# Kernel optimization log

Hardware: AMD Instinct MI355X
Metric: run time of the kernel (lower is better)

Reference implementation:

```python
import jax, jax.numpy as jnp
import numpy as np

B, L, D, H = 4, 2048, 1024, 16
d = D // H  # head_dim = 64
EPS = 1e-5
ROPE_BASE = 10000.0


def _rope_tables(seq_len, dim):
    inv_freq = 1.0 / (ROPE_BASE ** (jnp.arange(0, dim, 2, dtype=jnp.float32) / dim))
    t = jnp.arange(seq_len, dtype=jnp.float32)
    freqs = jnp.outer(t, inv_freq)                  # (L, d/2)
    emb = jnp.concatenate([freqs, freqs], axis=-1)  # (L, d)
    return jnp.cos(emb), jnp.sin(emb)


def _rotate_half(x):
    x1, x2 = jnp.split(x, 2, axis=-1)
    return jnp.concatenate([-x2, x1], axis=-1)


def setup_inputs() -> dict:
    key = jax.random.key(0)
    ks = jax.random.split(key, 5)
    x = jax.random.normal(ks[0], (B, L, D), dtype=jnp.float32)
    attn_mask = jnp.ones((B, 1, L, L), dtype=jnp.float32)
    conversion_mask = jax.random.uniform(ks[1], (B, L), dtype=jnp.float32)
    Wqkuv = jax.random.normal(ks[2], (D, 4 * D), dtype=jnp.float32) * (1.0 / np.sqrt(D))
    Wout = jax.random.normal(ks[3], (D, D), dtype=jnp.float32) * (1.0 / np.sqrt(D))
    ln_gamma = jnp.ones((d,), dtype=jnp.float32)
    ln_beta = jnp.zeros((d,), dtype=jnp.float32)
    conv_bias = jax.random.normal(ks[4], (H,), dtype=jnp.float32) * 0.02
    return {"x": x, "attn_mask": attn_mask, "conversion_mask": conversion_mask,
            "Wqkuv": Wqkuv, "Wout": Wout, "ln_gamma": ln_gamma,
            "ln_beta": ln_beta, "conv_bias": conv_bias}


def reference(x, attn_mask, conversion_mask, Wqkuv, Wout, ln_gamma, ln_beta, conv_bias):
    # qkuv projection with SiLU
    qkuv = jax.nn.silu(jnp.einsum('bld,de->ble', x, Wqkuv))  # (B, L, 4D)
    q, k, v, u = jnp.split(qkuv, 4, axis=-1)
    # reshape to (B, H, L, d)
    to_heads = lambda t: t.reshape(B, L, H, d).transpose(0, 2, 1, 3)
    q, k, v, u = map(to_heads, (q, k, v, u))
    # RoPE
    cos, sin = _rope_tables(L, d)            # (L, d)
    cos = cos[None, None]                    # (1,1,L,d)
    sin = sin[None, None]
    q = q * cos + _rotate_half(q) * sin
    k = k * cos + _rotate_half(k) * sin
    # scores + conversion bias + SiLU + multiplicative mask
    scores = jnp.einsum('bhld,bhmd->bhlm', q, k) / jnp.sqrt(jnp.float32(d))
    scores = scores + conversion_mask[:, None, None, :] * conv_bias[None, :, None, None]
    scores = jax.nn.silu(scores)
    scores = scores * attn_mask
    # attend, LayerNorm over head_dim, SiLU-gate with u
    attn_out = jnp.einsum('bhlm,bhmd->bhld', scores, v)
    mu = jnp.mean(attn_out, axis=-1, keepdims=True)
    var = jnp.var(attn_out, axis=-1, keepdims=True)
    attn_out = (attn_out - mu) / jnp.sqrt(var + EPS) * ln_gamma + ln_beta
    attn_out = attn_out * u
    attn_out = attn_out.transpose(0, 2, 1, 3).reshape(B, L, D)
    return jnp.einsum('bld,de->ble', attn_out, Wout)
```

## Files before the change

### kernel.cpp

```cpp
#include <hip/hip_runtime.h>
#include <math.h>
#include <stdint.h>

#define B_ 4
#define L_ 2048
#define D_ 1024
#define H_ 16

typedef __attribute__((ext_vector_type(4))) float f32x4;
typedef __attribute__((ext_vector_type(2))) float f32x2;
typedef __attribute__((ext_vector_type(8))) short s16x8;
typedef __attribute__((ext_vector_type(4))) short s16x4;
typedef __attribute__((ext_vector_type(4))) unsigned short u16x4;
typedef __attribute__((ext_vector_type(4))) unsigned int u32x4;
typedef __attribute__((ext_vector_type(2))) __bf16 bf16x2;

__device__ __forceinline__ unsigned short f2bf(float f) {
  unsigned int u = __float_as_uint(f);
  u += 0x7fffu + ((u >> 16) & 1u);
  return (unsigned short)(u >> 16);
}
__device__ __forceinline__ float b2f(unsigned short s) {
  return __uint_as_float(((unsigned int)s) << 16);
}
__device__ __forceinline__ unsigned int pk2(float a, float b) {
  f32x2 v;
  v[0] = a;
  v[1] = b;
  bf16x2 r = __builtin_convertvector(v, bf16x2);
  return __builtin_bit_cast(unsigned int, r);
}
__device__ __forceinline__ float silu_fast(float v) {
  return v * __builtin_amdgcn_rcpf(1.0f + __expf(-v));
}
__device__ __forceinline__ void gl_lds16(const void* g, void* l) {
  __builtin_amdgcn_global_load_lds(
      (__attribute__((address_space(1))) void*)(uintptr_t)g,
      (__attribute__((address_space(3))) void*)(uint32_t)(uintptr_t)l, 16, 0, 0);
}

__global__ __launch_bounds__(256) void conv_x(const float* __restrict__ x,
                                              unsigned short* __restrict__ xb, int n4) {
  int i = blockIdx.x * 256 + threadIdx.x;
  if (i < n4) {
    f32x4 v = *(const f32x4*)(x + (size_t)i * 4);
    u16x4 o;
#pragma unroll
    for (int j = 0; j < 4; ++j) o[j] = f2bf(v[j]);
    *(u16x4*)(xb + (size_t)i * 4) = o;
  }
}

__global__ __launch_bounds__(256) void trans_w(const float* __restrict__ W,
                                               unsigned short* __restrict__ Wt,
                                               int K, int N) {
  __shared__ float T[64][65];
  const int k0 = blockIdx.y * 64, n0 = blockIdx.x * 64;
  const int tid = threadIdx.x;
#pragma unroll
  for (int i = 0; i < 16; ++i) {
    int e = tid + i * 256;
    int r = e >> 6, c = e & 63;
    T[r][c] = W[(size_t)(k0 + r) * N + n0 + c];
  }
  __syncthreads();
#pragma unroll
  for (int i = 0; i < 16; ++i) {
    int e = tid + i * 256;
    int r = e >> 6, c = e & 63;
    Wt[(size_t)(n0 + r) * K + k0 + c] = f2bf(T[c][r]);
  }
}

__global__ __launch_bounds__(256) void rope_tab(f32x2* __restrict__ tab) {
  int i = blockIdx.x * 256 + threadIdx.x;
  int l = i >> 5, j = i & 31;
  float inv = expf(-(float)j * (9.210340371976184f / 32.0f));
  float ang = (float)l * inv;
  f32x2 cs;
  cs[0] = cosf(ang);
  cs[1] = sinf(ang);
  tab[i] = cs;
}

template <int MODE>
__global__ __launch_bounds__(256) void gemm_bf16(const unsigned short* __restrict__ A,
                                                 const unsigned short* __restrict__ Bt,
                                                 void* __restrict__ Cp,
                                                 int M, int N, int K) {
  alignas(16) __shared__ unsigned short As[128][32];
  alignas(16) __shared__ unsigned short Bs[128][32];
  const int tid = threadIdx.x;
  const int lane = tid & 63, w = tid >> 6;
  const int quad = lane >> 4, l15 = lane & 15;
  const int wr = w >> 1, wc = w & 1;
  const int m0 = blockIdx.y * 128, n0 = blockIdx.x * 128;
  const int srow = lane >> 2;
  const int schunk = (lane & 3) ^ ((lane >> 3) & 3);
  const int fcol = (quad ^ ((l15 >> 1) & 3)) * 8;
  f32x4 acc[4][4] = {};
  for (int k0 = 0; k0 < K; k0 += 32) {
    __syncthreads();
#pragma unroll
    for (int i = 0; i < 2; ++i) {
      int r0 = (w * 2 + i) * 16;
      gl_lds16(A + (size_t)(m0 + r0 + srow) * K + k0 + schunk * 8, &As[r0][0]);
      gl_lds16(Bt + (size_t)(n0 + r0 + srow) * K + k0 + schunk * 8, &Bs[r0][0]);
    }
    __syncthreads();
    s16x8 af[4], bf[4];
#pragma unroll
    for (int mi = 0; mi < 4; ++mi) af[mi] = *(const s16x8*)&As[wr * 64 + mi * 16 + l15][fcol];
#pragma unroll
    for (int nj = 0; nj < 4; ++nj) bf[nj] = *(const s16x8*)&Bs[wc * 64 + nj * 16 + l15][fcol];
#pragma unroll
    for (int mi = 0; mi < 4; ++mi)
#pragma unroll
      for (int nj = 0; nj < 4; ++nj)
        acc[mi][nj] = __builtin_amdgcn_mfma_f32_16x16x32_bf16(af[mi], bf[nj], acc[mi][nj], 0, 0, 0);
  }
#pragma unroll
  for (int mi = 0; mi < 4; ++mi)
#pragma unroll
    for (int nj = 0; nj < 4; ++nj)
#pragma unroll
      for (int reg = 0; reg < 4; ++reg) {
        int rg = m0 + wr * 64 + mi * 16 + quad * 4 + reg;
        int cg = n0 + wc * 64 + nj * 16 + l15;
        float v = acc[mi][nj][reg];
        if (MODE == 1) {
          ((unsigned short*)Cp)[(size_t)rg * N + cg] = f2bf(silu_fast(v));
        } else {
          ((float*)Cp)[(size_t)rg * N + cg] = v;
        }
      }
}

__global__ __launch_bounds__(256) void rope_conv(unsigned short* __restrict__ qk,
                                                 unsigned short* __restrict__ vt,
                                                 const f32x2* __restrict__ tab) {
  alignas(16) __shared__ unsigned short Vsh[64][72];
  const int tid = threadIdx.x;
  const int bh = blockIdx.y, b = bh >> 4, h = bh & 15;
  const int l0 = blockIdx.x * 64;
#pragma unroll
  for (int i = 0; i < 2; ++i) {
    int p = tid + i * 256;
    int row = p >> 3, c4 = p & 7;
    int l = l0 + row;
    size_t base = (size_t)(b * L_ + l) * 4096 + h * 64 + c4 * 4;
#pragma unroll
    for (int t = 0; t < 2; ++t) {
      size_t o = base + (size_t)t * 1024;
      u16x4 lo = *(u16x4*)(qk + o);
      u16x4 hi = *(u16x4*)(qk + o + 32);
      u16x4 nlo, nhi;
#pragma unroll
      for (int jj = 0; jj < 4; ++jj) {
        f32x2 cs = tab[l * 32 + c4 * 4 + jj];
        float fl = b2f(lo[jj]), fh = b2f(hi[jj]);
        nlo[jj] = f2bf(fl * cs[0] - fh * cs[1]);
        nhi[jj] = f2bf(fh * cs[0] + fl * cs[1]);
      }
      *(u16x4*)(qk + o) = nlo;
      *(u16x4*)(qk + o + 32) = nhi;
    }
  }
#pragma unroll
  for (int i = 0; i < 2; ++i) {
    int ch = tid + i * 256;
    int row = ch >> 3, c8 = ch & 7;
    *(s16x8*)&Vsh[row][c8 * 8] =
        *(const s16x8*)(qk + (size_t)(b * L_ + l0 + row) * 4096 + 2048 + h * 64 + c8 * 8);
  }
  __syncthreads();
#pragma unroll
  for (int i = 0; i < 2; ++i) {
    int ch = tid + i * 256;
    int drow = ch >> 3, c8 = ch & 7;
    s16x8 o;
#pragma unroll
    for (int jj = 0; jj < 8; ++jj) {
      int pos = c8 * 8 + jj;
      int g = pos >> 5, p = pos & 31;
      int lk = g * 32 + ((p >> 2) & 1) * 16 + ((p >> 3) & 3) * 4 + (p & 3);
      o[jj] = (short)Vsh[lk][drow];
    }
    *(s16x8*)(vt + (size_t)(bh * 64 + drow) * 2048 + l0 + c8 * 8) = o;
  }
}

__global__ __launch_bounds__(256) void attn_mfma(
    const unsigned short* __restrict__ qk, const unsigned short* __restrict__ vt,
    const float* __restrict__ amask, const float* __restrict__ cmask,
    const float* __restrict__ cbias, const float* __restrict__ gamma,
    const float* __restrict__ beta, unsigned short* __restrict__ attng) {
  alignas(16) __shared__ unsigned short Ks[64][64];
  alignas(16) __shared__ unsigned short Vts[64][64];
  const int tid = threadIdx.x;
  const int lane = tid & 63, w = tid >> 6;
  const int quad = lane >> 4, l15 = lane & 15;
  const int bh = blockIdx.y, b = bh >> 4, h = bh & 15;
  const int l0 = blockIdx.x * 128;
  const float cb = cbias[h];
  const int srow = lane >> 3;
  const int schunk = (lane & 7) ^ srow;

  s16x8 qf[2][2];
  const float* abase[2];
#pragma unroll
  for (int qs = 0; qs < 2; ++qs) {
    int qg = l0 + w * 32 + qs * 16 + l15;
#pragma unroll
    for (int s = 0; s < 2; ++s)
      qf[qs][s] = *(const s16x8*)(qk + (size_t)(b * L_ + qg) * 4096 + h * 64 + s * 32 + quad * 8);
    abase[qs] = amask + ((size_t)b * L_ + qg) * L_;
  }
  const float* cbase = cmask + (size_t)b * L_;

  f32x4 oacc[2][4] = {};

  for (int m0 = 0; m0 < L_; m0 += 64) {
    __syncthreads();
#pragma unroll
    for (int i = 0; i < 2; ++i) {
      int r0 = w * 16 + i * 8;
      gl_lds16(qk + (size_t)(b * L_ + m0 + r0 + srow) * 4096 + 1024 + h * 64 + schunk * 8,
               &Ks[r0][0]);
      gl_lds16(vt + (size_t)(bh * 64 + r0 + srow) * 2048 + m0 + schunk * 8, &Vts[r0][0]);
    }
    f32x4 cmcb[4], am4[2][4];
#pragma unroll
    for (int kt = 0; kt < 4; ++kt)
      cmcb[kt] = *(const f32x4*)(cbase + m0 + kt * 16 + quad * 4) * cb;
#pragma unroll
    for (int qs = 0; qs < 2; ++qs)
#pragma unroll
      for (int kt = 0; kt < 4; ++kt)
        am4[qs][kt] = *(const f32x4*)(abase[qs] + m0 + kt * 16 + quad * 4);
    __syncthreads();

    f32x4 sacc[2][4] = {};
#pragma unroll
    for (int s = 0; s < 2; ++s) {
      s16x8 kf[4];
#pragma unroll
      for (int kt = 0; kt < 4; ++kt)
        kf[kt] = *(const s16x8*)&Ks[kt * 16 + l15][((s * 4 + quad) ^ (l15 & 7)) * 8];
#pragma unroll
      for (int qs = 0; qs < 2; ++qs)
#pragma unroll
        for (int kt = 0; kt < 4; ++kt)
          sacc[qs][kt] = __builtin_amdgcn_mfma_f32_16x16x32_bf16(kf[kt], qf[qs][s],
                                                                 sacc[qs][kt], 0, 0, 0);
    }

    s16x8 pf[2][2];
#pragma unroll
    for (int qs = 0; qs < 2; ++qs)
#pragma unroll
      for (int t = 0; t < 2; ++t) {
        u32x4 pw;
#pragma unroll
        for (int half = 0; half < 2; ++half) {
          int kt = 2 * t + half;
          float x[4];
#pragma unroll
          for (int r = 0; r < 4; ++r) {
            float v = fmaf(sacc[qs][kt][r], 0.125f, cmcb[kt][r]);
            v = silu_fast(v);
            x[r] = v * am4[qs][kt][r];
          }
          pw[half * 2 + 0] = pk2(x[0], x[1]);
          pw[half * 2 + 1] = pk2(x[2], x[3]);
        }
        pf[qs][t] = __builtin_bit_cast(s16x8, pw);
      }

#pragma unroll
    for (int dt = 0; dt < 4; ++dt)
#pragma unroll
      for (int t = 0; t < 2; ++t) {
        s16x8 vf = *(const s16x8*)&Vts[dt * 16 + l15][((t * 4 + quad) ^ (l15 & 7)) * 8];
#pragma unroll
        for (int qs = 0; qs < 2; ++qs)
          oacc[qs][dt] = __builtin_amdgcn_mfma_f32_16x16x32_bf16(pf[qs][t], vf,
                                                                 oacc[qs][dt], 0, 0, 0);
      }
  }

#pragma unroll
  for (int qs = 0; qs < 2; ++qs) {
    float sm[4], sq[4];
#pragma unroll
    for (int reg = 0; reg < 4; ++reg) {
      float s1 = 0.f, s2 = 0.f;
#pragma unroll
      for (int dt = 0; dt < 4; ++dt) {
        float v = oacc[qs][dt][reg];
        s1 += v;
        s2 += v * v;
      }
      sm[reg] = s1;
      sq[reg] = s2;
    }
#pragma unroll
    for (int m = 1; m < 16; m <<= 1) {
#pragma unroll
      for (int reg = 0; reg < 4; ++reg) {
        sm[reg] += __shfl_xor(sm[reg], m);
        sq[reg] += __shfl_xor(sq[reg], m);
      }
    }
    float mu[4], rs[4];
#pragma unroll
    for (int reg = 0; reg < 4; ++reg) {
      mu[reg] = sm[reg] * (1.0f / 64.0f);
      float var = sq[reg] * (1.0f / 64.0f) - mu[reg] * mu[reg];
      rs[reg] = rsqrtf(var + 1e-5f);
    }
#pragma unroll
    for (int dt = 0; dt < 4; ++dt) {
      float g = gamma[dt * 16 + l15], be = beta[dt * 16 + l15];
#pragma unroll
      for (int reg = 0; reg < 4; ++reg) {
        int rowg = l0 + w * 32 + qs * 16 + quad * 4 + reg;
        int colg = dt * 16 + l15;
        float v = (oacc[qs][dt][reg] - mu[reg]) * rs[reg] * g + be;
        float u = b2f(qk[(size_t)(b * L_ + rowg) * 4096 + 3072 + h * 64 + colg]);
        attng[(size_t)(b * L_ + rowg) * 1024 + h * 64 + colg] = f2bf(v * u);
      }
    }
  }
}

extern "C" void kernel_launch(void* const* d_in, const int* in_sizes, int n_in,
                              void* d_out, int out_size, void* d_ws, size_t ws_size,
                              hipStream_t stream) {
  const float* x = (const float*)d_in[0];
  const float* amask = (const float*)d_in[1];
  const float* cmask = (const float*)d_in[2];
  const float* Wqkuv = (const float*)d_in[3];
  const float* Wout = (const float*)d_in[4];
  const float* gamma = (const float*)d_in[5];
  const float* beta = (const float*)d_in[6];
  const float* cbias = (const float*)d_in[7];
  float* out = (float*)d_out;

  char* ws = (char*)d_ws;
  unsigned short* qkuv_bf = (unsigned short*)ws;
  unsigned short* vt = (unsigned short*)(ws + ((size_t)64 << 20));
  unsigned short* xbf = (unsigned short*)(ws + ((size_t)80 << 20));
  unsigned short* Wt = (unsigned short*)(ws + ((size_t)96 << 20));
  unsigned short* Wot = (unsigned short*)(ws + ((size_t)104 << 20));
  unsigned short* attng = (unsigned short*)(ws + ((size_t)106 << 20));
  f32x2* tab = (f32x2*)(ws + ((size_t)122 << 20));

  conv_x<<<8192, 256, 0, stream>>>(x, xbf, (B_ * L_ * D_) / 4);
  trans_w<<<dim3(4096 / 64, 1024 / 64), 256, 0, stream>>>(Wqkuv, Wt, 1024, 4096);
  trans_w<<<dim3(1024 / 64, 1024 / 64), 256, 0, stream>>>(Wout, Wot, 1024, 1024);
  rope_tab<<<(L_ * 32) / 256, 256, 0, stream>>>(tab);

  gemm_bf16<1><<<dim3(4096 / 128, 8192 / 128), 256, 0, stream>>>(xbf, Wt, qkuv_bf,
                                                                 B_ * L_, 4 * D_, D_);
  rope_conv<<<dim3(L_ / 64, B_ * H_), 256, 0, stream>>>(qkuv_bf, vt, tab);
  attn_mfma<<<dim3(L_ / 128, B_ * H_), 256, 0, stream>>>(qkuv_bf, vt, amask, cmask, cbias,
                                                         gamma, beta, attng);
  gemm_bf16<0><<<dim3(1024 / 128, 8192 / 128), 256, 0, stream>>>(attng, Wot, out,
                                                                 B_ * L_, D_, D_);
}
```

Measured before the change: 462.6 us.

## Rewrite bf16 GEMM as 256x256 double-buffered tile with XCD swizzle and setprio

The GEMM moves from a 128x128 tile with BK=32 and 256 threads to a 256x256 tile with BK=64, 512 threads and double-buffered LDS. The next K tile is prefetched while MFMAs run, and workgroup IDs are swizzled across groups of eight for cache locality. s_setprio wraps the MFMA blocks in both the GEMM and the attention kernel. The goal is to hide global-load latency and raise MFMA utilisation, at the cost of more LDS (128KB) and registers. The output GEMM now launches only 128 blocks, which may underfill the GPU.

Measured after the change: 458.8 us. About the same (-0.8%).

```diff
diff --git a/kernel.cpp b/kernel.cpp
--- a/kernel.cpp
+++ b/kernel.cpp
@@ -84,50 +84,97 @@
 }
 
 template <int MODE>
-__global__ __launch_bounds__(256) void gemm_bf16(const unsigned short* __restrict__ A,
+__global__ __launch_bounds__(512) void gemm_bf16(const unsigned short* __restrict__ A,
                                                  const unsigned short* __restrict__ Bt,
                                                  void* __restrict__ Cp,
                                                  int M, int N, int K) {
-  alignas(16) __shared__ unsigned short As[128][32];
-  alignas(16) __shared__ unsigned short Bs[128][32];
+  alignas(16) __shared__ unsigned short Ash[2][256][64];
+  alignas(16) __shared__ unsigned short Bsh[2][256][64];
   const int tid = threadIdx.x;
   const int lane = tid & 63, w = tid >> 6;
   const int quad = lane >> 4, l15 = lane & 15;
-  const int wr = w >> 1, wc = w & 1;
-  const int m0 = blockIdx.y * 128, n0 = blockIdx.x * 128;
-  const int srow = lane >> 2;
-  const int schunk = (lane & 3) ^ ((lane >> 3) & 3);
-  const int fcol = (quad ^ ((l15 >> 1) & 3)) * 8;
-  f32x4 acc[4][4] = {};
-  for (int k0 = 0; k0 < K; k0 += 32) {
-    __syncthreads();
-#pragma unroll
-    for (int i = 0; i < 2; ++i) {
-      int r0 = (w * 2 + i) * 16;
-      gl_lds16(A + (size_t)(m0 + r0 + srow) * K + k0 + schunk * 8, &As[r0][0]);
-      gl_lds16(Bt + (size_t)(n0 + r0 + srow) * K + k0 + schunk * 8, &Bs[r0][0]);
-    }
-    __syncthreads();
-    s16x8 af[4], bf[4];
-#pragma unroll
-    for (int mi = 0; mi < 4; ++mi) af[mi] = *(const s16x8*)&As[wr * 64 + mi * 16 + l15][fcol];
-#pragma unroll
-    for (int nj = 0; nj < 4; ++nj) bf[nj] = *(const s16x8*)&Bs[wc * 64 + nj * 16 + l15][fcol];
-#pragma unroll
-    for (int mi = 0; mi < 4; ++mi)
-#pragma unroll
-      for (int nj = 0; nj < 4; ++nj)
-        acc[mi][nj] = __builtin_amdgcn_mfma_f32_16x16x32_bf16(af[mi], bf[nj], acc[mi][nj], 0, 0, 0);
-  }
-#pragma unroll
-  for (int mi = 0; mi < 4; ++mi)
-#pragma unroll
-    for (int nj = 0; nj < 4; ++nj)
+  const int wm = w >> 2, wn = w & 3;
+  const int nwg = gridDim.x * gridDim.y;
+  const int wgid = blockIdx.y * gridDim.x + blockIdx.x;
+  const int swz = (wgid & 7) * (nwg >> 3) + (wgid >> 3);
+  const int m0 = (swz / gridDim.x) * 256, n0 = (swz % gridDim.x) * 256;
+
+  const int s_sub = lane >> 3;
+  const int s_src = (lane & 7) ^ s_sub;
+  auto stage = [&](const unsigned short* __restrict__ G, int row0, int k0,
+                   unsigned short (*dst)[64]) {
+#pragma unroll
+    for (int j = 0; j < 4; ++j) {
+      int r = j * 64 + w * 8 + s_sub;
+      gl_lds16(G + (size_t)(row0 + r) * K + k0 + s_src * 8, &dst[j * 64 + w * 8][0]);
+    }
+  };
+
+  f32x4 acc[8][4] = {};
+  const int NT = K / 64;
+
+  stage(A, m0, 0, Ash[0]);
+  stage(Bt, n0, 0, Bsh[0]);
+  asm volatile("s_waitcnt vmcnt(0)" ::: "memory");
+  __builtin_amdgcn_s_barrier();
+  __builtin_amdgcn_sched_barrier(0);
+
+  for (int t = 0; t < NT; ++t) {
+    const int c = t & 1;
+#pragma unroll
+    for (int p = 0; p < 4; ++p) {
+      const int qa = p & 1, qb = p >> 1;
+      s16x8 af[4][2], bf[2][2];
+#pragma unroll
+      for (int i = 0; i < 4; ++i)
+#pragma unroll
+        for (int ks = 0; ks < 2; ++ks)
+          af[i][ks] = *(const s16x8*)&Ash[c][wm * 128 + (qa * 4 + i) * 16 + l15]
+                                           [((ks * 4 + quad) ^ (l15 & 7)) * 8];
+#pragma unroll
+      for (int jn = 0; jn < 2; ++jn)
+#pragma unroll
+        for (int ks = 0; ks < 2; ++ks)
+          bf[jn][ks] = *(const s16x8*)&Bsh[c][wn * 64 + (qb * 2 + jn) * 16 + l15]
+                                            [((ks * 4 + quad) ^ (l15 & 7)) * 8];
+      if (t + 1 < NT) {
+        if (p == 0) stage(A, m0, (t + 1) * 64, Ash[c ^ 1]);
+        if (p == 1) stage(Bt, n0, (t + 1) * 64, Bsh[c ^ 1]);
+      }
+      __builtin_amdgcn_sched_barrier(0);
+      __builtin_amdgcn_s_barrier();
+      __builtin_amdgcn_sched_barrier(0);
+      __builtin_amdgcn_s_setprio(1);
+#pragma unroll
+      for (int i = 0; i < 4; ++i)
+#pragma unroll
+        for (int jn = 0; jn < 2; ++jn)
+#pragma unroll
+          for (int ks = 0; ks < 2; ++ks)
+            acc[qa * 4 + i][qb * 2 + jn] = __builtin_amdgcn_mfma_f32_16x16x32_bf16(
+                af[i][ks], bf[jn][ks], acc[qa * 4 + i][qb * 2 + jn], 0, 0, 0);
+      __builtin_amdgcn_s_setprio(0);
+      if (p < 3) {
+        __builtin_amdgcn_s_barrier();
+        __builtin_amdgcn_sched_barrier(0);
+      }
+    }
+    if (t + 1 < NT) {
+      asm volatile("s_waitcnt vmcnt(0)" ::: "memory");
+    }
+    __builtin_amdgcn_s_barrier();
+    __builtin_amdgcn_sched_barrier(0);
+  }
+
+#pragma unroll
+  for (int fm = 0; fm < 8; ++fm)
+#pragma unroll
+    for (int fn = 0; fn < 4; ++fn)
 #pragma unroll
       for (int reg = 0; reg < 4; ++reg) {
-        int rg = m0 + wr * 64 + mi * 16 + quad * 4 + reg;
-        int cg = n0 + wc * 64 + nj * 16 + l15;
-        float v = acc[mi][nj][reg];
+        int rg = m0 + wm * 128 + fm * 16 + quad * 4 + reg;
+        int cg = n0 + wn * 64 + fn * 16 + l15;
+        float v = acc[fm][fn][reg];
         if (MODE == 1) {
           ((unsigned short*)Cp)[(size_t)rg * N + cg] = f2bf(silu_fast(v));
         } else {
@@ -247,12 +294,14 @@
 #pragma unroll
       for (int kt = 0; kt < 4; ++kt)
         kf[kt] = *(const s16x8*)&Ks[kt * 16 + l15][((s * 4 + quad) ^ (l15 & 7)) * 8];
+      __builtin_amdgcn_s_setprio(1);
 #pragma unroll
       for (int qs = 0; qs < 2; ++qs)
 #pragma unroll
         for (int kt = 0; kt < 4; ++kt)
           sacc[qs][kt] = __builtin_amdgcn_mfma_f32_16x16x32_bf16(kf[kt], qf[qs][s],
                                                                  sacc[qs][kt], 0, 0, 0);
+      __builtin_amdgcn_s_setprio(0);
     }
 
     s16x8 pf[2][2];
@@ -282,10 +331,12 @@
 #pragma unroll
       for (int t = 0; t < 2; ++t) {
         s16x8 vf = *(const s16x8*)&Vts[dt * 16 + l15][((t * 4 + quad) ^ (l15 & 7)) * 8];
+        __builtin_amdgcn_s_setprio(1);
 #pragma unroll
         for (int qs = 0; qs < 2; ++qs)
           oacc[qs][dt] = __builtin_amdgcn_mfma_f32_16x16x32_bf16(pf[qs][t], vf,
                                                                  oacc[qs][dt], 0, 0, 0);
+        __builtin_amdgcn_s_setprio(0);
       }
   }
 
@@ -361,11 +412,11 @@
   trans_w<<<dim3(1024 / 64, 1024 / 64), 256, 0, stream>>>(Wout, Wot, 1024, 1024);
   rope_tab<<<(L_ * 32) / 256, 256, 0, stream>>>(tab);
 
-  gemm_bf16<1><<<dim3(4096 / 128, 8192 / 128), 256, 0, stream>>>(xbf, Wt, qkuv_bf,
+  gemm_bf16<1><<<dim3(4096 / 256, 8192 / 256), 512, 0, stream>>>(xbf, Wt, qkuv_bf,
                                                                  B_ * L_, 4 * D_, D_);
   rope_conv<<<dim3(L_ / 64, B_ * H_), 256, 0, stream>>>(qkuv_bf, vt, tab);
   attn_mfma<<<dim3(L_ / 128, B_ * H_), 256, 0, stream>>>(qkuv_bf, vt, amask, cmask, cbias,
                                                          gamma, beta, attng);
-  gemm_bf16<0><<<dim3(1024 / 128, 8192 / 128), 256, 0, stream>>>(attng, Wot, out,
+  gemm_bf16<0><<<dim3(1024 / 256, 8192 / 256), 512, 0, stream>>>(attng, Wot, out,
                                                                  B_ * L_, D_, D_);
 }
```
